# Kernel tuning notes

Hardware: AMD Instinct MI355X
Metric: run time of the kernel (lower is better)

## Reference

```python
import jax, jax.numpy as jnp
import numpy as np

IN_CH = 32
OUT_CH = 32
N_NODES = 50000
BATCH = 16


def setup_inputs() -> dict:
    key = jax.random.key(0)
    kx, kw, kb = jax.random.split(key, 3)
    x = jax.random.normal(kx, (BATCH, IN_CH, N_NODES), dtype=jnp.float32)
    # per-node Conv1d(kernel_size=1) weights: [n, out, in], bias: [n, out]
    bound = 1.0 / np.sqrt(IN_CH)
    W = jax.random.uniform(kw, (N_NODES, OUT_CH, IN_CH), dtype=jnp.float32,
                           minval=-bound, maxval=bound)
    b = jax.random.uniform(kb, (N_NODES, OUT_CH), dtype=jnp.float32,
                           minval=-bound, maxval=bound)
    return {"x": x, "W": W, "b": b}


def reference(x, W, b):
    # fused locally connected 1x1 conv: out[b,o,n] = sum_h W[n,o,h]*x[b,h,n] + b[n,o]
    out = jnp.einsum('bhn,noh->bon', x, W)
    return out + b.T[None, :, :]  # b.T: [out, n]
```

## Files before the change

kernel.cpp:

```cpp
#include <hip/hip_runtime.h>


#define NN 50000
#define CH 32
#define NT 32
#define TPB 512
#define NXCD 8

typedef __attribute__((ext_vector_type(8))) short bf16x8;
typedef __attribute__((ext_vector_type(4))) float f32x4;
typedef __attribute__((ext_vector_type(4))) unsigned short bf16x4;
typedef float __attribute__((address_space(1))) gf32;
typedef float __attribute__((address_space(3))) lf32;

__device__ __forceinline__ unsigned short f2bf(float f) {
    union { float f; unsigned u; } v; v.f = f;
    return (unsigned short)((v.u + 0x7fffu + ((v.u >> 16) & 1u)) >> 16);
}

__global__ __launch_bounds__(TPB, 4)
void localconv1d_kernel(const float* __restrict__ x,
                        const float* __restrict__ W,
                        const float* __restrict__ bias,
                        float* __restrict__ out) {
    __shared__ __align__(16) char smem[69632];
    unsigned short* xs   = (unsigned short*)smem;
    char*           wlds = smem + 32768;
    float*          blds = (float*)(smem + 65536);
    float*          scr  = (float*)smem;

    const int tid  = threadIdx.x;
    const int lane = tid & 63;
    const int wv   = tid >> 6;
    const int bl   = lane & 15;
    const int hc   = lane >> 4;

    const int nwg  = (NN + NT - 1) / NT;
    const int q    = nwg / NXCD;
    const int r    = nwg % NXCD;
    const int orig = blockIdx.x;
    const int xcd  = orig % NXCD;
    const int wgid = (xcd < r ? xcd * (q + 1) : r * (q + 1) + (xcd - r) * q)
                     + orig / NXCD;
    int n0 = wgid * NT;
    if (n0 > NN - NT) n0 = NN - NT;

    if (wv < 4)
        __builtin_amdgcn_global_load_lds(
            (const gf32*)(bias + (size_t)n0 * CH + wv * 256 + lane * 4),
            (lf32*)(blds + wv * 256), 16, 0, 0);

    {
        const int chunk = tid & 7;
        float4 xv[2][4];
        #pragma unroll
        for (int u = 0; u < 2; ++u) {
            int gi = (tid >> 3) + u * 64;
            #pragma unroll
            for (int k = 0; k < 4; ++k) {
                int row = gi * 4 + k;
                xv[u][k] = *reinterpret_cast<const float4*>(
                    x + (size_t)row * NN + n0 + chunk * 4);
            }
        }
        #pragma unroll
        for (int u = 0; u < 2; ++u) {
            int gi = (tid >> 3) + u * 64;
            int b  = gi >> 3;
            int h4 = gi & 7;
            int hg = h4 >> 1;
            int jb = (h4 & 1) * 8;
            #pragma unroll
            for (int c = 0; c < 4; ++c) {
                int nn = chunk * 4 + c;
                unsigned base = (unsigned)(nn * 1024 + hg * 256 + b * 16 + jb);
                base ^= ((unsigned)(nn >> 2) & 7u) << 4;
                bf16x4 pk;
                pk[0] = f2bf(((const float*)&xv[u][0])[c]);
                pk[1] = f2bf(((const float*)&xv[u][1])[c]);
                pk[2] = f2bf(((const float*)&xv[u][2])[c]);
                pk[3] = f2bf(((const float*)&xv[u][3])[c]);
                *reinterpret_cast<bf16x4*>((char*)xs + base) = pk;
            }
        }
    }
    __syncthreads();

    const int lpermf = (lane * 4) ^ (((lane >> 3) & 7) << 2);
    #define ISSUE_W(s_)                                                          \
        do {                                                                     \
            int g_ = (s_) >> 1, H_ = (s_) & 1;                                   \
            const float* base_ = W + (size_t)(n0 + wv * 4 + g_) * 1024           \
                                 + H_ * 512;                                     \
            char* dst_ = wlds + wv * 4096 + ((s_) & 1) * 2048;                   \
            __builtin_amdgcn_global_load_lds((const gf32*)(base_ + lpermf),      \
                                             (lf32*)dst_, 16, 0, 2);             \
            __builtin_amdgcn_global_load_lds((const gf32*)(base_ + 256 + lpermf),\
                                             (lf32*)(dst_ + 1024), 16, 0, 2);    \
        } while (0)

    ISSUE_W(0);
    ISSUE_W(1);

    f32x4 acc[4][2];

    #pragma unroll
    for (int s = 0; s < 8; ++s) {
        if (s == 7) { asm volatile("s_waitcnt vmcnt(0)" ::: "memory"); }
        else        { asm volatile("s_waitcnt vmcnt(2)" ::: "memory"); }
        __builtin_amdgcn_sched_barrier(0);

        const int g  = s >> 1;
        const int Hh = s & 1;
        const int nn = wv * 4 + g;

        const char* wb = wlds + wv * 4096 + (s & 1) * 2048;
        const int slot0 = (bl * 8 + hc * 2) ^ (bl & 7);
        f32x4 wlo = *reinterpret_cast<const f32x4*>(wb + slot0 * 16);
        f32x4 whi = *reinterpret_cast<const f32x4*>(wb + (slot0 ^ 1) * 16);

        f32x4 cfr = *reinterpret_cast<const f32x4*>(blds + nn * 32 + 16 * Hh + 4 * hc);

        unsigned raddr = (unsigned)(nn * 1024 + lane * 16);
        raddr ^= ((unsigned)(nn >> 2) & 7u) << 4;
        bf16x8 bfrag = *reinterpret_cast<const bf16x8*>((const char*)xs + raddr);

        bf16x8 afrag;
        afrag[0] = f2bf(wlo[0]); afrag[1] = f2bf(wlo[1]);
        afrag[2] = f2bf(wlo[2]); afrag[3] = f2bf(wlo[3]);
        afrag[4] = f2bf(whi[0]); afrag[5] = f2bf(whi[1]);
        afrag[6] = f2bf(whi[2]); afrag[7] = f2bf(whi[3]);

        __builtin_amdgcn_sched_barrier(0);
        if (s + 2 < 8) ISSUE_W(s + 2);

        acc[g][Hh] = __builtin_amdgcn_mfma_f32_16x16x32_bf16(afrag, bfrag, cfr, 0, 0, 0);
    }

    __syncthreads();

    #pragma unroll
    for (int Hh = 0; Hh < 2; ++Hh) {
        #pragma unroll
        for (int bh = 0; bh < 2; ++bh) {
            if ((bl >> 3) == bh) {
                #pragma unroll
                for (int rr = 0; rr < 4; ++rr) {
                    int rp = (4 * hc + rr) * 8 + (bl & 7);
                    f32x4 v;
                    v[0] = acc[0][Hh][rr];
                    v[1] = acc[1][Hh][rr];
                    v[2] = acc[2][Hh][rr];
                    v[3] = acc[3][Hh][rr];
                    *reinterpret_cast<f32x4*>(scr + rp * 36 + wv * 4) = v;
                }
            }
            __syncthreads();
            #pragma unroll
            for (int it = 0; it < 2; ++it) {
                int R = it * 64 + (tid >> 3);
                int C = tid & 7;
                int o15 = R >> 3, B = R & 7;
                f32x4 v = *reinterpret_cast<const f32x4*>(scr + R * 36 + C * 4);
                f32x4* dst = reinterpret_cast<f32x4*>(
                    out + ((size_t)(bh * 8 + B) * CH + Hh * 16 + o15) * NN
                        + n0 + C * 4);
                __builtin_nontemporal_store(v, dst);
            }
            __syncthreads();
        }
    }
}

extern "C" void kernel_launch(void* const* d_in, const int* in_sizes, int n_in,
                              void* d_out, int out_size, void* d_ws, size_t ws_size,
                              hipStream_t stream) {
    const float* x    = (const float*)d_in[0];
    const float* W    = (const float*)d_in[1];
    const float* bias = (const float*)d_in[2];
    float* out        = (float*)d_out;

    const int blocks = (NN + NT - 1) / NT;
    localconv1d_kernel<<<blocks, TPB, 0, stream>>>(x, W, bias, out);
}
```

Measured before the change: 77.10 us.

## Preload x fragments into registers and deepen W prefetch to four stages

Each wave now loads all four of its bf16 x fragments from LDS into registers up front. It then reuses its own slice of the x staging area as two extra W buffers, which raises the number of in-flight W global-to-LDS loads from two steps to four. The epilogue scratch is moved to the W buffer region so it no longer overlaps the reused x area. The aim is to hide more of the global memory latency of the large streamed W tensor, at the cost of extra registers for the x fragments and explicit per-step waitcnt sequencing.

```diff
diff --git a/kernel.cpp b/kernel.cpp
--- a/kernel.cpp
+++ b/kernel.cpp
@@ -27,7 +27,7 @@
     unsigned short* xs   = (unsigned short*)smem;
     char*           wlds = smem + 32768;
     float*          blds = (float*)(smem + 65536);
-    float*          scr  = (float*)smem;
+    float*          scr  = (float*)(smem + 32768);
 
     const int tid  = threadIdx.x;
     const int lane = tid & 63;
@@ -86,56 +86,64 @@
     }
     __syncthreads();
 
+    bf16x8 bfr[4];
+    #pragma unroll
+    for (int g = 0; g < 4; ++g) {
+        int nn = wv * 4 + g;
+        unsigned ra = (unsigned)(nn * 1024 + lane * 16);
+        ra ^= ((unsigned)(nn >> 2) & 7u) << 4;
+        bfr[g] = *reinterpret_cast<const bf16x8*>((const char*)xs + ra);
+    }
+    asm volatile("s_waitcnt lgkmcnt(0)" ::: "memory");
+    __builtin_amdgcn_sched_barrier(0);
+
     const int lpermf = (lane * 4) ^ (((lane >> 3) & 7) << 2);
-    #define ISSUE_W(s_)                                                          \
-        do {                                                                     \
-            int g_ = (s_) >> 1, H_ = (s_) & 1;                                   \
-            const float* base_ = W + (size_t)(n0 + wv * 4 + g_) * 1024           \
-                                 + H_ * 512;                                     \
-            char* dst_ = wlds + wv * 4096 + ((s_) & 1) * 2048;                   \
-            __builtin_amdgcn_global_load_lds((const gf32*)(base_ + lpermf),      \
-                                             (lf32*)dst_, 16, 0, 2);             \
-            __builtin_amdgcn_global_load_lds((const gf32*)(base_ + 256 + lpermf),\
-                                             (lf32*)(dst_ + 1024), 16, 0, 2);    \
-        } while (0)
+#define WBUF(i_) ((((i_) & 3) < 2 ? wlds : (char*)xs) + wv * 4096 + ((i_) & 1) * 2048)
+#define ISSUE_W(s_)                                                          \
+    do {                                                                     \
+        const float* base_ = W + (size_t)(n0 + wv * 4 + ((s_) >> 1)) * 1024  \
+                             + ((s_) & 1) * 512;                             \
+        char* dst_ = WBUF(s_);                                               \
+        __builtin_amdgcn_global_load_lds((const gf32*)(base_ + lpermf),      \
+                                         (lf32*)dst_, 16, 0, 2);             \
+        __builtin_amdgcn_global_load_lds((const gf32*)(base_ + 256 + lpermf),\
+                                         (lf32*)(dst_ + 1024), 16, 0, 2);    \
+    } while (0)
 
-    ISSUE_W(0);
-    ISSUE_W(1);
+    ISSUE_W(0); ISSUE_W(1); ISSUE_W(2); ISSUE_W(3);
 
     f32x4 acc[4][2];
 
-    #pragma unroll
-    for (int s = 0; s < 8; ++s) {
-        if (s == 7) { asm volatile("s_waitcnt vmcnt(0)" ::: "memory"); }
-        else        { asm volatile("s_waitcnt vmcnt(2)" ::: "memory"); }
-        __builtin_amdgcn_sched_barrier(0);
+#define STEP(s_, v_)                                                          \
+    do {                                                                      \
+        asm volatile("s_waitcnt vmcnt(" #v_ ")" ::: "memory");                \
+        __builtin_amdgcn_sched_barrier(0);                                    \
+        const int g_ = (s_) >> 1, H_ = (s_) & 1;                              \
+        const int nn_ = wv * 4 + g_;                                          \
+        const char* wb_ = WBUF(s_);                                           \
+        const int slot_ = (bl * 8 + hc * 2) ^ (bl & 7);                       \
+        f32x4 wlo_ = *reinterpret_cast<const f32x4*>(wb_ + slot_ * 16);       \
+        f32x4 whi_ = *reinterpret_cast<const f32x4*>(wb_ + (slot_ ^ 1) * 16); \
+        f32x4 cfr_ = *reinterpret_cast<const f32x4*>(                         \
+            blds + nn_ * 32 + 16 * H_ + 4 * hc);                              \
+        bf16x8 af_;                                                           \
+        af_[0] = f2bf(wlo_[0]); af_[1] = f2bf(wlo_[1]);                       \
+        af_[2] = f2bf(wlo_[2]); af_[3] = f2bf(wlo_[3]);                       \
+        af_[4] = f2bf(whi_[0]); af_[5] = f2bf(whi_[1]);                       \
+        af_[6] = f2bf(whi_[2]); af_[7] = f2bf(whi_[3]);                       \
+        asm volatile("s_waitcnt lgkmcnt(0)" ::: "memory");                    \
+        __builtin_amdgcn_sched_barrier(0);                                    \
+        if ((s_) + 4 < 8) ISSUE_W((s_) + 4);                                  \
+        acc[g_][H_] = __builtin_amdgcn_mfma_f32_16x16x32_bf16(                \
+            af_, bfr[g_], cfr_, 0, 0, 0);                                     \
+    } while (0)
 
-        const int g  = s >> 1;
-        const int Hh = s & 1;
-        const int nn = wv * 4 + g;
+    STEP(0, 6); STEP(1, 6); STEP(2, 6); STEP(3, 6);
+    STEP(4, 6); STEP(5, 4); STEP(6, 2); STEP(7, 0);
 
-        const char* wb = wlds + wv * 4096 + (s & 1) * 2048;
-        const int slot0 = (bl * 8 + hc * 2) ^ (bl & 7);
-        f32x4 wlo = *reinterpret_cast<const f32x4*>(wb + slot0 * 16);
-        f32x4 whi = *reinterpret_cast<const f32x4*>(wb + (slot0 ^ 1) * 16);
-
-        f32x4 cfr = *reinterpret_cast<const f32x4*>(blds + nn * 32 + 16 * Hh + 4 * hc);
-
-        unsigned raddr = (unsigned)(nn * 1024 + lane * 16);
-        raddr ^= ((unsigned)(nn >> 2) & 7u) << 4;
-        bf16x8 bfrag = *reinterpret_cast<const bf16x8*>((const char*)xs + raddr);
-
-        bf16x8 afrag;
-        afrag[0] = f2bf(wlo[0]); afrag[1] = f2bf(wlo[1]);
-        afrag[2] = f2bf(wlo[2]); afrag[3] = f2bf(wlo[3]);
-        afrag[4] = f2bf(whi[0]); afrag[5] = f2bf(whi[1]);
-        afrag[6] = f2bf(whi[2]); afrag[7] = f2bf(whi[3]);
-
-        __builtin_amdgcn_sched_barrier(0);
-        if (s + 2 < 8) ISSUE_W(s + 2);
-
-        acc[g][Hh] = __builtin_amdgcn_mfma_f32_16x16x32_bf16(afrag, bfrag, cfr, 0, 0, 0);
-    }
+#undef STEP
+#undef ISSUE_W
+#undef WBUF
 
     __syncthreads();
 
```

After: 76.85 us. About the same (-0.3%).
